# Performance work log

Hardware: AMD Instinct MI355X
Metric: run time of the kernel (lower is better)

## Reference

```python
import jax, jax.numpy as jnp
import numpy as np
from jax import lax

BN_EPS = 1e-5


def setup_inputs() -> dict:
    key = jax.random.key(0)
    ks = jax.random.split(key, 12)
    h, c, i, kk = 8, 64, 96, 3
    c2, n, d = c // 2, 8, 512
    std = lambda f: np.float32(f)
    return {
        "X": jax.random.normal(ks[0], (h, n, d), jnp.float32),
        "lin_w": jax.random.normal(ks[1], (h, c2, d), jnp.float32) * std(d ** -0.5),
        "lin_b": jax.random.normal(ks[2], (h, c2), jnp.float32) * std(0.02),
        "bn_gamma": jnp.ones((h, c2), jnp.float32),
        "bn_beta": jnp.zeros((h, c2), jnp.float32),
        "px": jax.random.normal(ks[3], (1, 1, c2, 1, i), jnp.float32) * std(c ** -0.5),
        "py": jax.random.normal(ks[4], (1, 1, c2, i, 1), jnp.float32) * std(c ** -0.5),
        "kw": jax.random.normal(ks[5], (h, c, c), jnp.float32) * std(c ** -0.5),
        "kb": jax.random.normal(ks[6], (h, c), jnp.float32) * std(0.02),
        "vw": jax.random.normal(ks[7], (h, c, c), jnp.float32) * std(c ** -0.5),
        "vb": jax.random.normal(ks[8], (h, c), jnp.float32) * std(0.02),
        "sw": jax.random.normal(ks[9], (c, c, kk, kk), jnp.float32) * std((c * kk * kk) ** -0.5),
        "sb": jax.random.normal(ks[10], (c,), jnp.float32) * std(0.02),
    }


def reference(X, lin_w, lin_b, bn_gamma, bn_beta, px, py, kw, kb, vw, vb, sw, sb):
    h, n, _ = X.shape
    c = kw.shape[1]
    c2 = c // 2
    i = px.shape[-1]
    kk = sw.shape[-1]

    # --- MultiheadEmbedding: per-head Linear -> BatchNorm1d(train) -> ReLU ---
    y = jnp.einsum('hnd,hcd->hnc', X, lin_w) + lin_b[:, None, :]      # (h, n, c2)
    mu = y.mean(axis=1, keepdims=True)
    var = y.var(axis=1, keepdims=True)                                 # biased, as BN
    y = (y - mu) * lax.rsqrt(var + BN_EPS) * bn_gamma[:, None, :] + bn_beta[:, None, :]
    y = jax.nn.relu(y)
    M = jnp.transpose(y, (1, 0, 2))[..., None, None]                   # (n, h, c2, 1, 1)

    # --- PositionalEncoding: concat x/y translated copies -> (n, h, c, i, i) ---
    P = jnp.concatenate([
        jnp.broadcast_to(M + px, (n, h, c2, i, i)),
        jnp.broadcast_to(M + py, (n, h, c2, i, i)),
    ], axis=2)                                                          # (n, h, c, i, i)

    # --- TransposeAttention ---
    # grouped 1x1 key conv (groups = h)
    kp = jnp.einsum('nhcij,hdc->nhdij', P, kw) + kb[None, :, :, None, None]
    # score conv over each (c, i, i) map, shared across heads, scaled
    x = kp.reshape(n * h, c, i, i)
    s = lax.conv_general_dilated(x, sw, (1, 1), 'SAME',
                                 dimension_numbers=('NCHW', 'OIHW', 'NCHW'))
    s = (s + sb[None, :, None, None]) / np.float32((c * kk * kk) ** 0.5)
    w = jax.nn.softmax(s.reshape(n, h, c, i, i), axis=1)                # softmax over heads
    # grouped 1x1 value conv, weighted sum over heads
    vp = jnp.einsum('nhcij,hdc->nhdij', P, vw) + vb[None, :, :, None, None]
    T = (w * vp).sum(axis=1)                                            # (n, c, i, i)
    return (T, M, P, w)
```

## Files before the change

kernel.cpp:

```cpp
#include <hip/hip_runtime.h>
#include <math.h>

#define H    8
#define N    8
#define D    512
#define C    64
#define C2   32
#define I    96
#define II   9216

#define OFF_T 0
#define OFF_M 4718592
#define OFF_P 4720640
#define OFF_W 42469376

#define WS_AK    0
#define WS_AV    4096
#define WS_BV    8192
#define WS_CVT   57344
#define WS_BKT2  106496
#define WS_CKT2  157696
#define WS_SST   208896
#define WS_SPT   245760
#define WS_SQT   282624
#define WS_F     319488
#define WS_G2    356352
#define WS_H2    503808

__device__ __forceinline__ int bcls(int x) { return x == 0 ? 0 : (x == I - 1 ? 2 : 1); }

__global__ __launch_bounds__(256) void irf_embed(
    const float* __restrict__ X, const float* __restrict__ lin_w,
    const float* __restrict__ lin_b, const float* __restrict__ gamma,
    const float* __restrict__ beta, float* __restrict__ out)
{
    const int h = blockIdx.x, t = threadIdx.x;
    const int n = t >> 5, cc = t & 31;

    __shared__ float Xs[N * D];
    __shared__ float ys[N * C2];
    __shared__ float scale_s[C2], shift_s[C2];

    const float4* Xg  = (const float4*)(X + (size_t)h * N * D);
    float4*       Xs4 = (float4*)Xs;
    for (int idx = t; idx < N * D / 4; idx += 256) Xs4[idx] = Xg[idx];
    __syncthreads();

    const float4* wrow = (const float4*)(lin_w + ((size_t)h * C2 + cc) * D);
    const float4* xrow = (const float4*)(Xs + n * D);
    float a0 = 0.f, a1 = 0.f, a2 = 0.f, a3 = 0.f;
    #pragma unroll 4
    for (int k = 0; k < D / 4; ++k) {
        float4 xv = xrow[k], wv = wrow[k];
        a0 = fmaf(xv.x, wv.x, a0); a1 = fmaf(xv.y, wv.y, a1);
        a2 = fmaf(xv.z, wv.z, a2); a3 = fmaf(xv.w, wv.w, a3);
    }
    float y = (a0 + a1) + (a2 + a3) + lin_b[h * C2 + cc];
    ys[n * C2 + cc] = y;
    __syncthreads();

    if (t < C2) {
        float s = 0.f, ss = 0.f;
        #pragma unroll
        for (int j = 0; j < N; ++j) { float v = ys[j * C2 + t]; s += v; ss += v * v; }
        float mu  = s * (1.0f / N);
        float var = ss * (1.0f / N) - mu * mu;
        float sc  = rsqrtf(var + 1e-5f) * gamma[h * C2 + t];
        scale_s[t] = sc;
        shift_s[t] = beta[h * C2 + t] - mu * sc;
    }
    __syncthreads();

    float v = fmaxf(fmaf(y, scale_s[cc], shift_s[cc]), 0.0f);
    out[OFF_M + (n * H + h) * C2 + cc] = v;
}

__global__ __launch_bounds__(256) void irf_factors_a(
    const float* __restrict__ kw, const float* __restrict__ kb,
    const float* __restrict__ vw, const float* __restrict__ vb,
    const float* __restrict__ px, const float* __restrict__ py,
    const float* __restrict__ sw, const float* __restrict__ out,
    float* __restrict__ ws)
{
    int gid = blockIdx.x * 256 + threadIdx.x;
    if (gid < 4096) {
        int id = gid, d = id & 63, h = (id >> 6) & 7, n = id >> 9;
        const float* kwr = kw + ((size_t)h * C + d) * C;
        const float* vwr = vw + ((size_t)h * C + d) * C;
        const float* Mr  = out + OFF_M + (n * H + h) * C2;
        float ak = kb[h * C + d], av = vb[h * C + d];
        #pragma unroll 8
        for (int c = 0; c < C2; ++c) {
            float m = Mr[c];
            ak = fmaf(kwr[c] + kwr[C2 + c], m, ak);
            av = fmaf(vwr[c] + vwr[C2 + c], m, av);
        }
        ws[WS_AK + id] = ak;
        ws[WS_AV + id] = av;
    } else if (gid < 4096 + 49152) {
        int id = gid - 4096, d = id & 63, r = id >> 6, b = r % I, h = r / I;
        const float* kwr = kw + ((size_t)h * C + d) * C;
        const float* vwr = vw + ((size_t)h * C + d) * C;
        float bk = 0.f, bv = 0.f, ck = 0.f, cv = 0.f;
        #pragma unroll 8
        for (int c = 0; c < C2; ++c) {
            float pxv = px[c * I + b], pyv = py[c * I + b];
            bk = fmaf(kwr[c], pxv, bk);       bv = fmaf(vwr[c], pxv, bv);
            ck = fmaf(kwr[C2 + c], pyv, ck);  cv = fmaf(vwr[C2 + c], pyv, cv);
        }
        ws[WS_BKT2 + (h * C + d) * 100 + (b + 1)] = bk;
        ws[WS_BV   + (h * C + d) * I   + b]       = bv;
        ws[WS_CKT2 + (h * C + d) * 100 + (b + 1)] = ck;
        ws[WS_CVT  + (h * C + d) * I   + b]       = cv;
    } else if (gid < 4096 + 49152 + 4096) {
        int id = gid - (4096 + 49152), d = id & 63, e = id >> 6;
        float k9[3][3];
        const float* swr = sw + (size_t)(e * C + d) * 9;
        #pragma unroll
        for (int p = 0; p < 3; ++p)
            #pragma unroll
            for (int q = 0; q < 3; ++q) k9[p][q] = swr[p * 3 + q];
        #pragma unroll
        for (int ra = 0; ra < 3; ++ra) {
            int pmin = (ra == 0) ? 1 : 0, pmax = (ra == 2) ? 1 : 2;
            #pragma unroll
            for (int q = 0; q < 3; ++q) {
                float sp = 0.f;
                for (int p = pmin; p <= pmax; ++p) sp += k9[p][q];
                ws[WS_SPT + ((ra * 3 + q) * C + d) * C + e] = sp;
            }
            #pragma unroll
            for (int rb = 0; rb < 3; ++rb) {
                int qmin = (rb == 0) ? 1 : 0, qmax = (rb == 2) ? 1 : 2;
                float ssv = 0.f;
                for (int p = pmin; p <= pmax; ++p)
                    for (int q = qmin; q <= qmax; ++q) ssv += k9[p][q];
                ws[WS_SST + ((ra * 3 + rb) * C + d) * C + e] = ssv;
            }
        }
        #pragma unroll
        for (int rb = 0; rb < 3; ++rb) {
            int qmin = (rb == 0) ? 1 : 0, qmax = (rb == 2) ? 1 : 2;
            #pragma unroll
            for (int p = 0; p < 3; ++p) {
                float sq = 0.f;
                for (int q = qmin; q <= qmax; ++q) sq += k9[p][q];
                ws[WS_SQT + ((rb * 3 + p) * C + d) * C + e] = sq;
            }
        }
    } else {
        int s = gid - (4096 + 49152 + 4096);
        int d = s & 63, h = (s >> 6) & 7, k = s >> 9;
        int col = (k & 3) == 0 ? 0 : 96 + (k & 3);
        int base = (k >> 2) ? WS_CKT2 : WS_BKT2;
        ws[base + (h * C + d) * 100 + col] = 0.f;
    }
}

__global__ __launch_bounds__(256) void irf_factors_b(float* __restrict__ ws)
{
    int gid = blockIdx.x * 256 + threadIdx.x;
    if (gid < 36864) {
        int e = gid & 63, h = (gid >> 6) & 7, cls = (gid >> 9) % 9, n = gid / 4608;
        const float* ak  = ws + WS_AK + (n * H + h) * C;
        const float* sst = ws + WS_SST + cls * (C * C) + e;
        float acc = 0.f;
        #pragma unroll 8
        for (int d = 0; d < C; ++d) acc = fmaf(ak[d], sst[d * C], acc);
        ws[WS_F + gid] = acc;
    } else if (gid < 73728) {
        int j = gid - 36864;
        int b4 = j % 24, e = (j / 24) & 63, h = (j / 1536) & 7, ra = j / 12288;
        const float* sp  = ws + WS_SPT + (ra * 3) * (C * C) + e;
        const float* row = ws + WS_BKT2 + h * (C * 100) + 4 * b4;
        float4 acc = make_float4(0.f, 0.f, 0.f, 0.f);
        #pragma unroll 4
        for (int d = 0; d < C; ++d) {
            float s0 = sp[d * C], s1 = sp[4096 + d * C], s2 = sp[8192 + d * C];
            float4 A = *(const float4*)(row + d * 100);
            float4 B = *(const float4*)(row + d * 100 + 4);
            acc.x = fmaf(s0, A.x, fmaf(s1, A.y, fmaf(s2, A.z, acc.x)));
            acc.y = fmaf(s0, A.y, fmaf(s1, A.z, fmaf(s2, A.w, acc.y)));
            acc.z = fmaf(s0, A.z, fmaf(s1, A.w, fmaf(s2, B.x, acc.z)));
            acc.w = fmaf(s0, A.w, fmaf(s1, B.x, fmaf(s2, B.y, acc.w)));
        }
        ((float4*)(ws + WS_G2 + ((ra * H + h) * C + e) * I))[b4] = acc;
    } else {
        int j = gid - 73728;
        int a4 = j % 24, e = (j / 24) & 63, h = (j / 1536) & 7, rb = j / 12288;
        const float* sq  = ws + WS_SQT + (rb * 3) * (C * C) + e;
        const float* row = ws + WS_CKT2 + h * (C * 100) + 4 * a4;
        float4 acc = make_float4(0.f, 0.f, 0.f, 0.f);
        #pragma unroll 4
        for (int d = 0; d < C; ++d) {
            float s0 = sq[d * C], s1 = sq[4096 + d * C], s2 = sq[8192 + d * C];
            float4 A = *(const float4*)(row + d * 100);
            float4 B = *(const float4*)(row + d * 100 + 4);
            acc.x = fmaf(s0, A.x, fmaf(s1, A.y, fmaf(s2, A.z, acc.x)));
            acc.y = fmaf(s0, A.y, fmaf(s1, A.z, fmaf(s2, A.w, acc.y)));
            acc.z = fmaf(s0, A.z, fmaf(s1, A.w, fmaf(s2, B.x, acc.z)));
            acc.w = fmaf(s0, A.w, fmaf(s1, B.x, fmaf(s2, B.y, acc.w)));
        }
        ((float4*)(ws + WS_H2 + ((rb * H + h) * C + e) * I))[a4] = acc;
    }
}

__global__ __launch_bounds__(256) void irf_softmax(
    const float* __restrict__ sb, const float* __restrict__ ws,
    float* __restrict__ out)
{
    const int bid = blockIdx.x;
    const int n = bid >> 6, e = bid & 63;
    const int t = threadIdx.x;

    __shared__ __align__(16) float G2s[3 * H * I];
    __shared__ __align__(16) float H2s[3 * H * I];
    __shared__ __align__(16) float BVs[H * I];
    __shared__ float CVs[H * I];
    __shared__ float Fs[9 * H];
    __shared__ float AVs[H];

    for (int o = t; o < 3 * H * I; o += 256) {
        int rh = o / I, sp = o - rh * I;
        G2s[o] = ws[WS_G2 + (rh * C + e) * I + sp];
        H2s[o] = ws[WS_H2 + (rh * C + e) * I + sp];
    }
    for (int o = t; o < H * I; o += 256) {
        int h = o / I, sp = o - h * I;
        BVs[o] = ws[WS_BV  + (h * C + e) * I + sp];
        CVs[o] = ws[WS_CVT + (h * C + e) * I + sp];
    }
    if (t < 9 * H) Fs[t] = ws[WS_F + ((n * 9 + t / 8) * H + (t & 7)) * C + e];
    if (t < H)     AVs[t] = ws[WS_AV + (n * H + t) * C + e];
    const float sbv = sb[e];
    __syncthreads();

    const float inv24 = 1.0f / 24.0f;
    float4* Tplane = (float4*)(out + OFF_T + (size_t)(n * C + e) * II);

    #pragma unroll
    for (int it = 0; it < 9; ++it) {
        int idx = it * 256 + t;
        int a = idx / 24, b4 = idx - a * 24;
        int ra = bcls(a);

        float4 sv[H];
        float4 mx = make_float4(-1e30f, -1e30f, -1e30f, -1e30f);
        #pragma unroll
        for (int h = 0; h < H; ++h) {
            float4 g2 = ((const float4*)(G2s + (ra * H + h) * I))[b4];
            float f1 = Fs[(ra * 3 + 1) * H + h] + H2s[(H + h) * I + a] + sbv;
            float fx = f1, fw = f1;
            if (b4 == 0)  fx = Fs[(ra * 3 + 0) * H + h] + H2s[h * I + a] + sbv;
            if (b4 == 23) fw = Fs[(ra * 3 + 2) * H + h] + H2s[(2 * H + h) * I + a] + sbv;
            float4 s;
            s.x = (fx + g2.x) * inv24;
            s.y = (f1 + g2.y) * inv24;
            s.z = (f1 + g2.z) * inv24;
            s.w = (fw + g2.w) * inv24;
            sv[h] = s;
            mx.x = fmaxf(mx.x, s.x); mx.y = fmaxf(mx.y, s.y);
            mx.z = fmaxf(mx.z, s.z); mx.w = fmaxf(mx.w, s.w);
        }
        float4 sum = make_float4(0.f, 0.f, 0.f, 0.f);
        #pragma unroll
        for (int h = 0; h < H; ++h) {
            sv[h].x = __expf(sv[h].x - mx.x); sum.x += sv[h].x;
            sv[h].y = __expf(sv[h].y - mx.y); sum.y += sv[h].y;
            sv[h].z = __expf(sv[h].z - mx.z); sum.z += sv[h].z;
            sv[h].w = __expf(sv[h].w - mx.w); sum.w += sv[h].w;
        }
        float4 rs;
        rs.x = 1.0f / sum.x; rs.y = 1.0f / sum.y;
        rs.z = 1.0f / sum.z; rs.w = 1.0f / sum.w;

        float4 T = make_float4(0.f, 0.f, 0.f, 0.f);
        #pragma unroll
        for (int h = 0; h < H; ++h) {
            float4 w;
            w.x = sv[h].x * rs.x; w.y = sv[h].y * rs.y;
            w.z = sv[h].z * rs.z; w.w = sv[h].w * rs.w;
            ((float4*)(out + OFF_W + (size_t)((n * H + h) * C + e) * II))[idx] = w;
            float ac = AVs[h] + CVs[h * I + a];
            float4 bv = ((const float4*)(BVs + h * I))[b4];
            T.x = fmaf(w.x, ac + bv.x, T.x);
            T.y = fmaf(w.y, ac + bv.y, T.y);
            T.z = fmaf(w.z, ac + bv.z, T.z);
            T.w = fmaf(w.w, ac + bv.w, T.w);
        }
        Tplane[idx] = T;
    }
}

__global__ __launch_bounds__(256) void irf_pwrite(
    const float* __restrict__ px, const float* __restrict__ py,
    float* __restrict__ out)
{
    const int bid = blockIdx.x;
    const int c = bid & 63, nh = bid >> 6;
    const int t = threadIdx.x;

    __shared__ __align__(16) float rowp[I];
    const float m = out[OFF_M + nh * C2 + (c & 31)];
    if (t < I / 4) {
        const float* src = (c < C2) ? (px + c * I) : (py + (c - C2) * I);
        ((float4*)rowp)[t] = ((const float4*)src)[t];
    }
    __syncthreads();

    float4* plane = (float4*)(out + OFF_P + (size_t)bid * II);
    if (c < C2) {
        #pragma unroll
        for (int it = 0; it < 9; ++it) {
            int idx = it * 256 + t;
            float4 v = ((const float4*)rowp)[idx % 24];
            v.x += m; v.y += m; v.z += m; v.w += m;
            plane[idx] = v;
        }
    } else {
        #pragma unroll
        for (int it = 0; it < 9; ++it) {
            int idx = it * 256 + t;
            float vv = m + rowp[idx / 24];
            plane[idx] = make_float4(vv, vv, vv, vv);
        }
    }
}

extern "C" void kernel_launch(void* const* d_in, const int* in_sizes, int n_in,
                              void* d_out, int out_size, void* d_ws, size_t ws_size,
                              hipStream_t stream) {
    const float* X     = (const float*)d_in[0];
    const float* lin_w = (const float*)d_in[1];
    const float* lin_b = (const float*)d_in[2];
    const float* gamma = (const float*)d_in[3];
    const float* beta  = (const float*)d_in[4];
    const float* px    = (const float*)d_in[5];
    const float* py    = (const float*)d_in[6];
    const float* kw    = (const float*)d_in[7];
    const float* kb    = (const float*)d_in[8];
    const float* vw    = (const float*)d_in[9];
    const float* vb    = (const float*)d_in[10];
    const float* sw    = (const float*)d_in[11];
    const float* sb    = (const float*)d_in[12];

    float* out = (float*)d_out;
    float* ws  = (float*)d_ws;

    irf_embed    <<<8,    256, 0, stream>>>(X, lin_w, lin_b, gamma, beta, out);
    irf_factors_a<<<240,  256, 0, stream>>>(kw, kb, vw, vb, px, py, sw, out, ws);
    irf_factors_b<<<432,  256, 0, stream>>>(ws);
    irf_softmax  <<<512,  256, 0, stream>>>(sb, ws, out);
    irf_pwrite   <<<4096, 256, 0, stream>>>(px, py, out);
}
```

Measured before the change: 392.9 us.

## Merge softmax and P-write kernels into one launch with nontemporal stores

Fuses the softmax/T kernel and the P-broadcast writer into a single launch whose blocks branch on block index. The softmax part is also split three ways per (n,e) plane, giving 1536 blocks instead of 512 for better occupancy. Shared-memory staging now uses float4 loads, and all large output writes use nontemporal stores to avoid polluting cache. The cost is that each softmax block reloads the same per-(e) factor tables, so the staging reads are tripled, and the shared-memory footprint is sized for the larger branch across all blocks.

```diff
diff --git a/kernel.cpp b/kernel.cpp
--- a/kernel.cpp
+++ b/kernel.cpp
@@ -8,6 +8,12 @@
 #define C2   32
 #define I    96
 #define II   9216
+
+typedef float floatx4 __attribute__((ext_vector_type(4)));
+__device__ __forceinline__ void nt_store4(float4 v, float4* p) {
+    floatx4 r; r.x = v.x; r.y = v.y; r.z = v.z; r.w = v.w;
+    __builtin_nontemporal_store(r, (floatx4*)p);
+}
 
 #define OFF_T 0
 #define OFF_M 4718592
@@ -205,124 +211,129 @@
     }
 }
 
-__global__ __launch_bounds__(256) void irf_softmax(
+__global__ __launch_bounds__(256) void irf_out(
+    const float* __restrict__ px, const float* __restrict__ py,
     const float* __restrict__ sb, const float* __restrict__ ws,
     float* __restrict__ out)
 {
     const int bid = blockIdx.x;
-    const int n = bid >> 6, e = bid & 63;
     const int t = threadIdx.x;
 
-    __shared__ __align__(16) float G2s[3 * H * I];
-    __shared__ __align__(16) float H2s[3 * H * I];
-    __shared__ __align__(16) float BVs[H * I];
-    __shared__ float CVs[H * I];
-    __shared__ float Fs[9 * H];
-    __shared__ float AVs[H];
-
-    for (int o = t; o < 3 * H * I; o += 256) {
-        int rh = o / I, sp = o - rh * I;
-        G2s[o] = ws[WS_G2 + (rh * C + e) * I + sp];
-        H2s[o] = ws[WS_H2 + (rh * C + e) * I + sp];
-    }
-    for (int o = t; o < H * I; o += 256) {
-        int h = o / I, sp = o - h * I;
-        BVs[o] = ws[WS_BV  + (h * C + e) * I + sp];
-        CVs[o] = ws[WS_CVT + (h * C + e) * I + sp];
-    }
-    if (t < 9 * H) Fs[t] = ws[WS_F + ((n * 9 + t / 8) * H + (t & 7)) * C + e];
-    if (t < H)     AVs[t] = ws[WS_AV + (n * H + t) * C + e];
-    const float sbv = sb[e];
-    __syncthreads();
-
-    const float inv24 = 1.0f / 24.0f;
-    float4* Tplane = (float4*)(out + OFF_T + (size_t)(n * C + e) * II);
-
-    #pragma unroll
-    for (int it = 0; it < 9; ++it) {
-        int idx = it * 256 + t;
-        int a = idx / 24, b4 = idx - a * 24;
-        int ra = bcls(a);
-
-        float4 sv[H];
-        float4 mx = make_float4(-1e30f, -1e30f, -1e30f, -1e30f);
-        #pragma unroll
-        for (int h = 0; h < H; ++h) {
-            float4 g2 = ((const float4*)(G2s + (ra * H + h) * I))[b4];
-            float f1 = Fs[(ra * 3 + 1) * H + h] + H2s[(H + h) * I + a] + sbv;
-            float fx = f1, fw = f1;
-            if (b4 == 0)  fx = Fs[(ra * 3 + 0) * H + h] + H2s[h * I + a] + sbv;
-            if (b4 == 23) fw = Fs[(ra * 3 + 2) * H + h] + H2s[(2 * H + h) * I + a] + sbv;
-            float4 s;
-            s.x = (fx + g2.x) * inv24;
-            s.y = (f1 + g2.y) * inv24;
-            s.z = (f1 + g2.z) * inv24;
-            s.w = (fw + g2.w) * inv24;
-            sv[h] = s;
-            mx.x = fmaxf(mx.x, s.x); mx.y = fmaxf(mx.y, s.y);
-            mx.z = fmaxf(mx.z, s.z); mx.w = fmaxf(mx.w, s.w);
-        }
-        float4 sum = make_float4(0.f, 0.f, 0.f, 0.f);
-        #pragma unroll
-        for (int h = 0; h < H; ++h) {
-            sv[h].x = __expf(sv[h].x - mx.x); sum.x += sv[h].x;
-            sv[h].y = __expf(sv[h].y - mx.y); sum.y += sv[h].y;
-            sv[h].z = __expf(sv[h].z - mx.z); sum.z += sv[h].z;
-            sv[h].w = __expf(sv[h].w - mx.w); sum.w += sv[h].w;
-        }
-        float4 rs;
-        rs.x = 1.0f / sum.x; rs.y = 1.0f / sum.y;
-        rs.z = 1.0f / sum.z; rs.w = 1.0f / sum.w;
-
-        float4 T = make_float4(0.f, 0.f, 0.f, 0.f);
-        #pragma unroll
-        for (int h = 0; h < H; ++h) {
-            float4 w;
-            w.x = sv[h].x * rs.x; w.y = sv[h].y * rs.y;
-            w.z = sv[h].z * rs.z; w.w = sv[h].w * rs.w;
-            ((float4*)(out + OFF_W + (size_t)((n * H + h) * C + e) * II))[idx] = w;
-            float ac = AVs[h] + CVs[h * I + a];
-            float4 bv = ((const float4*)(BVs + h * I))[b4];
-            T.x = fmaf(w.x, ac + bv.x, T.x);
-            T.y = fmaf(w.y, ac + bv.y, T.y);
-            T.z = fmaf(w.z, ac + bv.z, T.z);
-            T.w = fmaf(w.w, ac + bv.w, T.w);
-        }
-        Tplane[idx] = T;
-    }
-}
-
-__global__ __launch_bounds__(256) void irf_pwrite(
-    const float* __restrict__ px, const float* __restrict__ py,
-    float* __restrict__ out)
-{
-    const int bid = blockIdx.x;
-    const int c = bid & 63, nh = bid >> 6;
-    const int t = threadIdx.x;
-
-    __shared__ __align__(16) float rowp[I];
-    const float m = out[OFF_M + nh * C2 + (c & 31)];
-    if (t < I / 4) {
-        const float* src = (c < C2) ? (px + c * I) : (py + (c - C2) * I);
-        ((float4*)rowp)[t] = ((const float4*)src)[t];
-    }
-    __syncthreads();
-
-    float4* plane = (float4*)(out + OFF_P + (size_t)bid * II);
-    if (c < C2) {
-        #pragma unroll
-        for (int it = 0; it < 9; ++it) {
-            int idx = it * 256 + t;
-            float4 v = ((const float4*)rowp)[idx % 24];
-            v.x += m; v.y += m; v.z += m; v.w += m;
-            plane[idx] = v;
+    if (bid < 1536) {
+        const int n = bid / 192, rem = bid - n * 192;
+        const int e = rem / 3, slice = rem - e * 3;
+
+        __shared__ __align__(16) float G2s[3 * H * I];
+        __shared__ __align__(16) float H2s[3 * H * I];
+        __shared__ __align__(16) float BVs[H * I];
+        __shared__ __align__(16) float CVs[H * I];
+        __shared__ float Fs[9 * H];
+        __shared__ float AVs[H];
+
+        {
+            float4* G2s4 = (float4*)G2s; float4* H2s4 = (float4*)H2s;
+            const int R4 = I / 4;
+            for (int o = t; o < 3 * H * R4; o += 256) {
+                int rh = o / R4, sp4 = o - rh * R4;
+                G2s4[o] = ((const float4*)(ws + WS_G2 + (rh * C + e) * I))[sp4];
+                H2s4[o] = ((const float4*)(ws + WS_H2 + (rh * C + e) * I))[sp4];
+            }
+            float4* BVs4 = (float4*)BVs; float4* CVs4 = (float4*)CVs;
+            for (int o = t; o < H * R4; o += 256) {
+                int h = o / R4, sp4 = o - h * R4;
+                BVs4[o] = ((const float4*)(ws + WS_BV  + (h * C + e) * I))[sp4];
+                CVs4[o] = ((const float4*)(ws + WS_CVT + (h * C + e) * I))[sp4];
+            }
+            if (t < 9 * H) Fs[t] = ws[WS_F + ((n * 9 + t / 8) * H + (t & 7)) * C + e];
+            if (t < H)     AVs[t] = ws[WS_AV + (n * H + t) * C + e];
+        }
+        const float sbv = sb[e];
+        __syncthreads();
+
+        const float inv24 = 1.0f / 24.0f;
+        float4* Tplane = (float4*)(out + OFF_T + (size_t)(n * C + e) * II);
+
+        #pragma unroll
+        for (int it = 0; it < 3; ++it) {
+            int local = it * 256 + t;
+            int a = slice * 32 + local / 24, b4 = local % 24;
+            int idx = a * 24 + b4;
+            int ra = bcls(a);
+
+            float4 sv[H];
+            float4 mx = make_float4(-1e30f, -1e30f, -1e30f, -1e30f);
+            #pragma unroll
+            for (int h = 0; h < H; ++h) {
+                float4 g2 = ((const float4*)(G2s + (ra * H + h) * I))[b4];
+                float f1 = Fs[(ra * 3 + 1) * H + h] + H2s[(H + h) * I + a] + sbv;
+                float fx = f1, fw = f1;
+                if (b4 == 0)  fx = Fs[(ra * 3 + 0) * H + h] + H2s[h * I + a] + sbv;
+                if (b4 == 23) fw = Fs[(ra * 3 + 2) * H + h] + H2s[(2 * H + h) * I + a] + sbv;
+                float4 s;
+                s.x = (fx + g2.x) * inv24;
+                s.y = (f1 + g2.y) * inv24;
+                s.z = (f1 + g2.z) * inv24;
+                s.w = (fw + g2.w) * inv24;
+                sv[h] = s;
+                mx.x = fmaxf(mx.x, s.x); mx.y = fmaxf(mx.y, s.y);
+                mx.z = fmaxf(mx.z, s.z); mx.w = fmaxf(mx.w, s.w);
+            }
+            float4 sum = make_float4(0.f, 0.f, 0.f, 0.f);
+            #pragma unroll
+            for (int h = 0; h < H; ++h) {
+                sv[h].x = __expf(sv[h].x - mx.x); sum.x += sv[h].x;
+                sv[h].y = __expf(sv[h].y - mx.y); sum.y += sv[h].y;
+                sv[h].z = __expf(sv[h].z - mx.z); sum.z += sv[h].z;
+                sv[h].w = __expf(sv[h].w - mx.w); sum.w += sv[h].w;
+            }
+            float4 rs;
+            rs.x = 1.0f / sum.x; rs.y = 1.0f / sum.y;
+            rs.z = 1.0f / sum.z; rs.w = 1.0f / sum.w;
+
+            float4 T = make_float4(0.f, 0.f, 0.f, 0.f);
+            #pragma unroll
+            for (int h = 0; h < H; ++h) {
+                float4 w;
+                w.x = sv[h].x * rs.x; w.y = sv[h].y * rs.y;
+                w.z = sv[h].z * rs.z; w.w = sv[h].w * rs.w;
+                nt_store4(w, ((float4*)(out + OFF_W + (size_t)((n * H + h) * C + e) * II)) + idx);
+                float ac = AVs[h] + CVs[h * I + a];
+                float4 bv = ((const float4*)(BVs + h * I))[b4];
+                T.x = fmaf(w.x, ac + bv.x, T.x);
+                T.y = fmaf(w.y, ac + bv.y, T.y);
+                T.z = fmaf(w.z, ac + bv.z, T.z);
+                T.w = fmaf(w.w, ac + bv.w, T.w);
+            }
+            nt_store4(T, Tplane + idx);
         }
     } else {
-        #pragma unroll
-        for (int it = 0; it < 9; ++it) {
-            int idx = it * 256 + t;
-            float vv = m + rowp[idx / 24];
-            plane[idx] = make_float4(vv, vv, vv, vv);
+        const int pb = bid - 1536;
+        const int c = pb & 63, nh = pb >> 6;
+
+        __shared__ __align__(16) float rowp[I];
+        const float m = out[OFF_M + nh * C2 + (c & 31)];
+        if (t < I / 4) {
+            const float* src = (c < C2) ? (px + c * I) : (py + (c - C2) * I);
+            ((float4*)rowp)[t] = ((const float4*)src)[t];
+        }
+        __syncthreads();
+
+        float4* plane = (float4*)(out + OFF_P + (size_t)pb * II);
+        if (c < C2) {
+            #pragma unroll
+            for (int it = 0; it < 9; ++it) {
+                int idx = it * 256 + t;
+                float4 v = ((const float4*)rowp)[idx % 24];
+                v.x += m; v.y += m; v.z += m; v.w += m;
+                nt_store4(v, plane + idx);
+            }
+        } else {
+            #pragma unroll
+            for (int it = 0; it < 9; ++it) {
+                int idx = it * 256 + t;
+                float vv = m + rowp[idx / 24];
+                nt_store4(make_float4(vv, vv, vv, vv), plane + idx);
+            }
         }
     }
 }
@@ -350,6 +361,5 @@
     irf_embed    <<<8,    256, 0, stream>>>(X, lin_w, lin_b, gamma, beta, out);
     irf_factors_a<<<240,  256, 0, stream>>>(kw, kb, vw, vb, px, py, sw, out, ws);
     irf_factors_b<<<432,  256, 0, stream>>>(ws);
-    irf_softmax  <<<512,  256, 0, stream>>>(sb, ws, out);
-    irf_pwrite   <<<4096, 256, 0, stream>>>(px, py, out);
-}
+    irf_out      <<<5632, 256, 0, stream>>>(px, py, sb, ws, out);
+}
```

Measured after the change: 396.3 us. About the same (+0.9%).
